# Kernel tuning notes

Hardware: AMD Instinct MI355X
Metric: run time of the kernel (lower is better)

Reference implementation:

```python
import jax, jax.numpy as jnp
import numpy as np

N, H, W = 512, 256, 256


def setup_inputs() -> dict:
    key = jax.random.key(0)
    k1, k2, k3, k4 = jax.random.split(key, 4)
    means3D = jax.random.normal(k1, (N, 3), dtype=jnp.float32) * 2.0
    A = jax.random.normal(k2, (N, 3, 3), dtype=jnp.float32) * 0.1
    covs3d = jnp.einsum('nij,nkj->nik', A, A) + 1e-4 * jnp.eye(3, dtype=jnp.float32)
    colors = jax.random.uniform(k3, (N, 3), dtype=jnp.float32)
    opacities = jax.random.uniform(k4, (N,), dtype=jnp.float32)
    fx = fy = 500.0
    K = jnp.array([[fx, 0.0, W / 2.0], [0.0, fy, H / 2.0], [0.0, 0.0, 1.0]], dtype=jnp.float32)
    R = jnp.eye(3, dtype=jnp.float32)
    t = jnp.array([0.0, 0.0, 10.0], dtype=jnp.float32)
    y, x = jnp.meshgrid(jnp.arange(H, dtype=jnp.float32), jnp.arange(W, dtype=jnp.float32), indexing='ij')
    pixels = jnp.stack([x, y], axis=-1)  # [H, W, 2]
    return dict(means3D=means3D, covs3d=covs3d, colors=colors, opacities=opacities, K=K, R=R, t=t, pixels=pixels)


def reference(means3D, covs3d, colors, opacities, K, R, t, pixels):
    # --- projection ---
    cam = means3D @ R.T + t[None, :]            # [N,3]
    depths = jnp.clip(cam[:, 2], 1.0)           # clamp(min=1.0)
    screen = cam @ K.T
    means2D = screen[:, :2] / screen[:, 2:3]    # [N,2]
    fx, fy = K[0, 0], K[1, 1]
    X, Y, Z = cam[:, 0], cam[:, 1], cam[:, 2]
    zeros = jnp.zeros_like(Z)
    # Jacobian of perspective projection, [N,2,3]
    J = jnp.stack([
        jnp.stack([fx / Z, zeros, -fx * X / (Z * Z)], axis=-1),
        jnp.stack([zeros, fy / Z, -fy * Y / (Z * Z)], axis=-1),
    ], axis=1)
    covs_cam = jnp.einsum('ij,njk,lk->nil', R, covs3d, R)     # R C R^T
    covs2D = jnp.einsum('nij,njk,nlk->nil', J, covs_cam, J)   # [N,2,2]

    # --- depth sort + validity ---
    valid = (depths > 1.0) & (depths < 50.0)
    idx = jnp.argsort(depths)
    means2D = means2D[idx]
    covs2D = covs2D[idx]
    colors_s = colors[idx]
    opac_s = opacities[idx]
    valid = valid[idx]

    # --- per-pixel gaussian values (explicit 2x2 inverse/det) ---
    covs2D = covs2D + 1e-4 * jnp.eye(2, dtype=covs2D.dtype)
    a, b = covs2D[:, 0, 0], covs2D[:, 0, 1]
    c, d = covs2D[:, 1, 0], covs2D[:, 1, 1]
    det = a * d - b * c
    ia, ib, ic, id_ = d / det, -b / det, -c / det, a / det
    dx = pixels[None, :, :, :] - means2D[:, None, None, :]    # [N,H,W,2]
    dx0, dx1 = dx[..., 0], dx[..., 1]
    expo = -0.5 * (ia[:, None, None] * dx0 * dx0
                   + (ib + ic)[:, None, None] * dx0 * dx1
                   + id_[:, None, None] * dx1 * dx1)
    norm = 1.0 / (2.0 * jnp.pi * jnp.sqrt(det))
    gauss = norm[:, None, None] * jnp.exp(expo)               # [N,H,W]
    gauss = gauss * valid[:, None, None].astype(gauss.dtype)

    # --- alpha compositing front-to-back ---
    alphas = opac_s[:, None, None] * gauss                    # [N,H,W]
    T = jnp.cumprod(1.0 - alphas, axis=0)
    T = jnp.concatenate([jnp.ones((1, H, W), dtype=alphas.dtype), T[:-1]], axis=0)
    weights = alphas * T
    rendered = jnp.einsum('nhw,nc->hwc', weights, colors_s)   # [H,W,3]
    return rendered
```

## Files before the change

### kernel.cpp

```cpp
#include <hip/hip_runtime.h>
#include <math.h>

#define N_G   512
#define W_IMG 256
#define H_IMG 256


__global__ __launch_bounds__(512) void project_sort_kernel(
    const float* __restrict__ means3D, const float* __restrict__ covs3d,
    const float* __restrict__ colors,  const float* __restrict__ opac,
    const float* __restrict__ Km, const float* __restrict__ Rm,
    const float* __restrict__ tv, float4* __restrict__ params_out)
{
    __shared__ float  s_key[N_G];
    __shared__ int    s_ord[N_G];
    __shared__ float4 s_par[N_G * 3];

    const int t = threadIdx.x;

    const float R00=Rm[0],R01=Rm[1],R02=Rm[2],
                R10=Rm[3],R11=Rm[4],R12=Rm[5],
                R20=Rm[6],R21=Rm[7],R22=Rm[8];
    const float K00=Km[0],K01=Km[1],K02=Km[2],
                K10=Km[3],K11=Km[4],K12=Km[5],
                K20=Km[6],K21=Km[7],K22=Km[8];
    const float t0=tv[0],t1=tv[1],t2=tv[2];

    const float m0=means3D[3*t], m1=means3D[3*t+1], m2=means3D[3*t+2];
    const float cx = R00*m0 + R01*m1 + R02*m2 + t0;
    const float cy = R10*m0 + R11*m1 + R12*m2 + t1;
    const float cz = R20*m0 + R21*m1 + R22*m2 + t2;
    const float depth = fmaxf(cz, 1.0f);

    const float s0 = K00*cx + K01*cy + K02*cz;
    const float s1 = K10*cx + K11*cy + K12*cz;
    const float s2 = K20*cx + K21*cy + K22*cz;
    const float mx = s0 / s2;
    const float my = s1 / s2;

    const float C00=covs3d[9*t+0], C01=covs3d[9*t+1], C02=covs3d[9*t+2];
    const float C10=covs3d[9*t+3], C11=covs3d[9*t+4], C12=covs3d[9*t+5];
    const float C20=covs3d[9*t+6], C21=covs3d[9*t+7], C22=covs3d[9*t+8];

    float T00 = R00*C00 + R01*C10 + R02*C20;
    float T01 = R00*C01 + R01*C11 + R02*C21;
    float T02 = R00*C02 + R01*C12 + R02*C22;
    float T10 = R10*C00 + R11*C10 + R12*C20;
    float T11 = R10*C01 + R11*C11 + R12*C21;
    float T12 = R10*C02 + R11*C12 + R12*C22;
    float T20 = R20*C00 + R21*C10 + R22*C20;
    float T21 = R20*C01 + R21*C11 + R22*C21;
    float T22 = R20*C02 + R21*C12 + R22*C22;

    const float cc00 = T00*R00 + T01*R01 + T02*R02;
    const float cc01 = T00*R10 + T01*R11 + T02*R12;
    const float cc02 = T00*R20 + T01*R21 + T02*R22;
    const float cc10 = T10*R00 + T11*R01 + T12*R02;
    const float cc11 = T10*R10 + T11*R11 + T12*R12;
    const float cc12 = T10*R20 + T11*R21 + T12*R22;
    const float cc20 = T20*R00 + T21*R01 + T22*R02;
    const float cc21 = T20*R10 + T21*R11 + T22*R12;
    const float cc22 = T20*R20 + T21*R21 + T22*R22;

    const float fx = K00, fy = K11;
    const float invz = 1.0f / cz;
    const float J00 = fx * invz;
    const float J02 = -fx * cx * invz * invz;
    const float J11 = fy * invz;
    const float J12 = -fy * cy * invz * invz;

    const float U00 = J00*cc00 + J02*cc20;
    const float U01 = J00*cc01 + J02*cc21;
    const float U02 = J00*cc02 + J02*cc22;
    const float U10 = J11*cc10 + J12*cc20;
    const float U11 = J11*cc11 + J12*cc21;
    const float U12 = J11*cc12 + J12*cc22;

    const float a = U00*J00 + U02*J02 + 1e-4f;
    const float b = U01*J11 + U02*J12;
    const float c = U10*J00 + U12*J02;
    const float d = U11*J11 + U12*J12 + 1e-4f;

    const float det = a*d - b*c;
    const float ia  = d / det;
    const float id_ = a / det;
    const float sib = (b + c) / det;

    const float qa = -0.5f * ia;
    const float qb =  0.5f * sib;
    const float qd = -0.5f * id_;

    const bool valid = (depth > 1.0f) && (depth < 50.0f);
    const float norm = 0.15915494309189535f * rsqrtf(det) * (det > 0.f ? 1.f : 1.f);
    float w = valid ? opac[t] * norm : 0.0f;
    if (!(w > 0.0f)) w = 0.0f;

    const float hm  = 0.5f * (ia + id_);
    const float dh  = 0.5f * (ia - id_);
    const float off = 0.5f * sib;
    const float lmin = hm - sqrtf(dh*dh + off*off);

    float r2cut;
    if (w <= 1e-9f)        r2cut = -1.0f;
    else if (lmin <= 0.f)  r2cut = 1e30f;
    else                   r2cut = 2.0f * __logf(w * 1e9f) / lmin;

    s_key[t] = depth;
    s_ord[t] = t;
    s_par[t*3+0] = make_float4(mx, my, qa, qb);
    s_par[t*3+1] = make_float4(qd, w, r2cut, colors[3*t]);
    s_par[t*3+2] = make_float4(colors[3*t+1], colors[3*t+2], 0.f, 0.f);
    __syncthreads();

    for (int k = 2; k <= N_G; k <<= 1) {
        for (int j = k >> 1; j > 0; j >>= 1) {
            const int ixj = t ^ j;
            if (ixj > t) {
                const float ka = s_key[t], kb = s_key[ixj];
                const int   oa = s_ord[t], ob = s_ord[ixj];
                const bool up   = ((t & k) == 0);
                const bool agtb = (ka > kb) || (ka == kb && oa > ob);
                if (agtb == up) {
                    s_key[t] = kb; s_key[ixj] = ka;
                    s_ord[t] = ob; s_ord[ixj] = oa;
                }
            }
            __syncthreads();
        }
    }

    const int gi = s_ord[t];
    params_out[t*3+0] = s_par[gi*3+0];
    params_out[t*3+1] = s_par[gi*3+1];
    params_out[t*3+2] = s_par[gi*3+2];
}

__global__ __launch_bounds__(256) void render_kernel(
    const float4* __restrict__ params, float* __restrict__ out)
{
    __shared__ int    s_cnt[8];
    __shared__ int    s_off[9];
    __shared__ int    s_idx[N_G];
    __shared__ float4 s_p[N_G * 3];

    const int tid  = threadIdx.x;
    const int wave = tid >> 6;
    const int lane = tid & 63;
    const int x0 = blockIdx.x * 16;
    const int y0 = blockIdx.y * 16;
    const float rx0 = (float)x0, ry0 = (float)y0;
    const float rx1 = rx0 + 15.f, ry1 = ry0 + 15.f;

    bool pass[2];
    unsigned long long mm[2];
    int gix[2];
    #pragma unroll
    for (int cgrp = 0; cgrp < 2; ++cgrp) {
        const int g = wave + 4 * cgrp;
        const int i = g * 64 + lane;
        gix[cgrp] = i;
        const float4 p0 = params[i*3];
        const float4 p1 = params[i*3+1];
        const float w = p1.y, r2cut = p1.z;
        const float cxp = fminf(fmaxf(p0.x, rx0), rx1);
        const float cyp = fminf(fmaxf(p0.y, ry0), ry1);
        const float ddx = p0.x - cxp, ddy = p0.y - cyp;
        const float d2 = ddx*ddx + ddy*ddy;
        pass[cgrp] = (w > 0.f) && (d2 <= r2cut);
        mm[cgrp] = __ballot(pass[cgrp]);
        if (lane == 0) s_cnt[g] = __popcll(mm[cgrp]);
    }
    __syncthreads();
    if (tid == 0) {
        int acc = 0;
        for (int g = 0; g < 8; ++g) { s_off[g] = acc; acc += s_cnt[g]; }
        s_off[8] = acc;
    }
    __syncthreads();
    #pragma unroll
    for (int cgrp = 0; cgrp < 2; ++cgrp) {
        const int g = wave + 4 * cgrp;
        if (pass[cgrp]) {
            const int rank = __popcll(mm[cgrp] & ((1ull << lane) - 1ull));
            s_idx[s_off[g] + rank] = gix[cgrp];
        }
    }
    __syncthreads();
    const int count = s_off[8];

    for (int j = tid; j < count; j += 256) {
        const int gi = s_idx[j];
        s_p[j*3+0] = params[gi*3+0];
        s_p[j*3+1] = params[gi*3+1];
        s_p[j*3+2] = params[gi*3+2];
    }
    __syncthreads();

    const float px = (float)(x0 + (tid & 15));
    const float py = (float)(y0 + (tid >> 4));
    float T = 1.f, accr = 0.f, accg = 0.f, accb = 0.f;

    #pragma unroll 2
    for (int j = 0; j < count; ++j) {
        const float4 p0 = s_p[j*3+0];
        const float4 p1 = s_p[j*3+1];
        const float4 p2 = s_p[j*3+2];
        const float dx = px - p0.x;
        const float dy = py - p0.y;
        const float e = (p0.z*dx + p0.w*dy)*dx + p1.x*dy*dy;
        const float alpha = p1.y * __expf(e);
        const float wt = alpha * T;
        accr = fmaf(wt, p1.w, accr);
        accg = fmaf(wt, p2.x, accg);
        accb = fmaf(wt, p2.y, accb);
        T *= (1.f - alpha);
    }

    const int o = ((y0 + (tid >> 4)) * W_IMG + (x0 + (tid & 15))) * 3;
    out[o+0] = accr;
    out[o+1] = accg;
    out[o+2] = accb;
}

extern "C" void kernel_launch(void* const* d_in, const int* in_sizes, int n_in,
                              void* d_out, int out_size, void* d_ws, size_t ws_size,
                              hipStream_t stream) {
    const float* means3D = (const float*)d_in[0];
    const float* covs3d  = (const float*)d_in[1];
    const float* colors  = (const float*)d_in[2];
    const float* opac    = (const float*)d_in[3];
    const float* Km      = (const float*)d_in[4];
    const float* Rm      = (const float*)d_in[5];
    const float* tv      = (const float*)d_in[6];

    float4* params = (float4*)d_ws;
    float*  out    = (float*)d_out;

    hipLaunchKernelGGL(project_sort_kernel, dim3(1), dim3(512), 0, stream,
                       means3D, covs3d, colors, opac, Km, Rm, tv, params);
    hipLaunchKernelGGL(render_kernel, dim3(16, 16), dim3(256), 0, stream,
                       params, out);
}
```

Measured before the change: 84.21 us.

## Replace bitonic sort with rank-by-counting scatter and loosen gaussian cutoff

The projection kernel no longer runs a 45-stage bitonic sort with barriers between stages. Each thread instead computes its rank by counting smaller depth keys, compared as float bits since depths are positive, and breaks ties by index. It then writes its parameters straight to the sorted slot, which removes the shared staging buffer and the many __syncthreads. The culling threshold moves from 1e-9 to 1e-7, which drops more faint contributions per tile at a small accuracy cost. The render loop unroll goes from 2 to 4 and the transmittance update becomes a single fma.

```diff
diff --git a/kernel.cpp b/kernel.cpp
--- a/kernel.cpp
+++ b/kernel.cpp
@@ -6,15 +6,13 @@
 #define H_IMG 256
 
 
-__global__ __launch_bounds__(512) void project_sort_kernel(
+__global__ __launch_bounds__(512) void gs_project_rank(
     const float* __restrict__ means3D, const float* __restrict__ covs3d,
     const float* __restrict__ colors,  const float* __restrict__ opac,
     const float* __restrict__ Km, const float* __restrict__ Rm,
     const float* __restrict__ tv, float4* __restrict__ params_out)
 {
-    __shared__ float  s_key[N_G];
-    __shared__ int    s_ord[N_G];
-    __shared__ float4 s_par[N_G * 3];
+    __shared__ unsigned int s_key[N_G];
 
     const int t = threadIdx.x;
 
@@ -91,7 +89,7 @@
     const float qd = -0.5f * id_;
 
     const bool valid = (depth > 1.0f) && (depth < 50.0f);
-    const float norm = 0.15915494309189535f * rsqrtf(det) * (det > 0.f ? 1.f : 1.f);
+    const float norm = 0.15915494309189535f * rsqrtf(det);
     float w = valid ? opac[t] * norm : 0.0f;
     if (!(w > 0.0f)) w = 0.0f;
 
@@ -101,41 +99,30 @@
     const float lmin = hm - sqrtf(dh*dh + off*off);
 
     float r2cut;
-    if (w <= 1e-9f)        r2cut = -1.0f;
+    if (w <= 1e-7f)        r2cut = -1.0f;
     else if (lmin <= 0.f)  r2cut = 1e30f;
-    else                   r2cut = 2.0f * __logf(w * 1e9f) / lmin;
-
-    s_key[t] = depth;
-    s_ord[t] = t;
-    s_par[t*3+0] = make_float4(mx, my, qa, qb);
-    s_par[t*3+1] = make_float4(qd, w, r2cut, colors[3*t]);
-    s_par[t*3+2] = make_float4(colors[3*t+1], colors[3*t+2], 0.f, 0.f);
-    __syncthreads();
-
-    for (int k = 2; k <= N_G; k <<= 1) {
-        for (int j = k >> 1; j > 0; j >>= 1) {
-            const int ixj = t ^ j;
-            if (ixj > t) {
-                const float ka = s_key[t], kb = s_key[ixj];
-                const int   oa = s_ord[t], ob = s_ord[ixj];
-                const bool up   = ((t & k) == 0);
-                const bool agtb = (ka > kb) || (ka == kb && oa > ob);
-                if (agtb == up) {
-                    s_key[t] = kb; s_key[ixj] = ka;
-                    s_ord[t] = ob; s_ord[ixj] = oa;
-                }
-            }
-            __syncthreads();
-        }
-    }
-
-    const int gi = s_ord[t];
-    params_out[t*3+0] = s_par[gi*3+0];
-    params_out[t*3+1] = s_par[gi*3+1];
-    params_out[t*3+2] = s_par[gi*3+2];
+    else                   r2cut = 2.0f * __logf(w * 1e7f) / lmin;
+
+    const unsigned int kb = __float_as_uint(depth);
+    s_key[t] = kb;
+    __syncthreads();
+
+    int rank = 0;
+    const uint4* k4 = (const uint4*)s_key;
+    #pragma unroll 4
+    for (int j = 0; j < N_G / 4; ++j) {
+        const uint4 k = k4[j];
+        rank += (k.x < kb) + (k.y < kb) + (k.z < kb) + (k.w < kb);
+    }
+    for (int j = 0; j < t; ++j)
+        rank += (s_key[j] == kb);
+
+    params_out[rank*3+0] = make_float4(mx, my, qa, qb);
+    params_out[rank*3+1] = make_float4(qd, w, r2cut, colors[3*t]);
+    params_out[rank*3+2] = make_float4(colors[3*t+1], colors[3*t+2], 0.f, 0.f);
 }
 
-__global__ __launch_bounds__(256) void render_kernel(
+__global__ __launch_bounds__(256) void gs_render(
     const float4* __restrict__ params, float* __restrict__ out)
 {
     __shared__ int    s_cnt[8];
@@ -200,7 +187,7 @@
     const float py = (float)(y0 + (tid >> 4));
     float T = 1.f, accr = 0.f, accg = 0.f, accb = 0.f;
 
-    #pragma unroll 2
+    #pragma unroll 4
     for (int j = 0; j < count; ++j) {
         const float4 p0 = s_p[j*3+0];
         const float4 p1 = s_p[j*3+1];
@@ -213,7 +200,7 @@
         accr = fmaf(wt, p1.w, accr);
         accg = fmaf(wt, p2.x, accg);
         accb = fmaf(wt, p2.y, accb);
-        T *= (1.f - alpha);
+        T = fmaf(-alpha, T, T);
     }
 
     const int o = ((y0 + (tid >> 4)) * W_IMG + (x0 + (tid & 15))) * 3;
@@ -236,8 +223,8 @@
     float4* params = (float4*)d_ws;
     float*  out    = (float*)d_out;
 
-    hipLaunchKernelGGL(project_sort_kernel, dim3(1), dim3(512), 0, stream,
+    hipLaunchKernelGGL(gs_project_rank, dim3(1), dim3(512), 0, stream,
                        means3D, covs3d, colors, opac, Km, Rm, tv, params);
-    hipLaunchKernelGGL(render_kernel, dim3(16, 16), dim3(256), 0, stream,
+    hipLaunchKernelGGL(gs_render, dim3(16, 16), dim3(256), 0, stream,
                        params, out);
 }
```

Result: no change. 84.18 us (-0.0%).
